# Kernel optimization log

Hardware: AMD Instinct MI355X
Metric: run time of the kernel (lower is better)

## Reference

```python
import jax, jax.numpy as jnp
import numpy as np

BITWIDTH = 4  # sqllm 4-bit packing: 8 codes per int32


def sqllm_dequant4(qweight, lut):
    # qweight: [num_int32s, N] int32 (stored packed); lut: [N, 16]
    qw = qweight.T  # [N, num_int32s]
    shifts = jnp.arange(8, dtype=jnp.int32) * 4  # [8]
    # extract 8 nibbles per int32 -> indices in [0, 16)
    idx = (qw[:, :, None] >> shifts[None, None, :]) & 15  # [N, num_int32s, 8]
    N = qw.shape[0]
    idx = idx.reshape(N, -1)  # [N, K] with K = num_int32s * 8
    return jnp.take_along_axis(lut, idx, axis=1)  # [N, K]


def setup_inputs() -> dict:
    key = jax.random.key(0)
    k1, k2, k3 = jax.random.split(key, 3)
    B, S, K, N = 4, 2048, 4096, 4096
    inp = {
        "input": jax.random.normal(k1, (B, S, K), dtype=jnp.float32),
        "qweight": jax.random.randint(k2, (K // 8, N), 0, 2147483647, dtype=jnp.int32),
        "lut": jax.random.normal(k3, (N, 16), dtype=jnp.float32),
    }
    return inp


def reference(input, qweight, lut):
    # sqllm_gemm: dequantize packed 4-bit weights via LUT gather, then input @ W.T
    weights = sqllm_dequant4(qweight, lut)  # [N, K]
    return jnp.einsum("bsk,nk->bsn", input, weights)  # [B, S, N]
```

## Files before the change

### kernel.cpp

```cpp
#include <hip/hip_runtime.h>
#include <hip/hip_bf16.h>


typedef __attribute__((ext_vector_type(4))) float  f32x4;
typedef __attribute__((ext_vector_type(4))) int    i32x4;
typedef __attribute__((ext_vector_type(8))) short  bf16x8;

__device__ __forceinline__ unsigned short f2bf(float f) {
    __hip_bfloat16 h = __float2bfloat16(f);
    return __builtin_bit_cast(unsigned short, h);
}

__device__ __forceinline__ void gload16(const unsigned short* g, unsigned short* l) {
    __builtin_amdgcn_global_load_lds(
        (const __attribute__((address_space(1))) unsigned int*)g,
        (__attribute__((address_space(3))) unsigned int*)l, 16, 0, 0);
}


__global__ void convA_kernel(const float* __restrict__ in, unsigned short* __restrict__ o, long n8) {
    long i = (long)blockIdx.x * blockDim.x + threadIdx.x;
    long stride = (long)gridDim.x * blockDim.x;
    const f32x4* in4 = reinterpret_cast<const f32x4*>(in);
    bf16x8* o8 = reinterpret_cast<bf16x8*>(o);
    for (; i < n8; i += stride) {
        f32x4 a = in4[2 * i];
        f32x4 b = in4[2 * i + 1];
        bf16x8 e;
#pragma unroll
        for (int x = 0; x < 4; ++x) {
            e[x]     = (short)f2bf(a[x]);
            e[4 + x] = (short)f2bf(b[x]);
        }
        o8[i] = e;
    }
}

__global__ void dequantW_kernel(const int* __restrict__ Q, const float* __restrict__ lut,
                                unsigned short* __restrict__ Wb, int N, long total) {
    long i = (long)blockIdx.x * blockDim.x + threadIdx.x;
    if (i >= total) return;
    unsigned int v = (unsigned int)Q[i];
    int n = (int)(i % N);
    const float* lp = lut + (long)n * 16;
    bf16x8 w;
#pragma unroll
    for (int p = 0; p < 8; ++p)
        w[p] = (short)f2bf(lp[(v >> (4 * p)) & 15]);
    reinterpret_cast<bf16x8*>(Wb)[i] = w;
}


#define MFMA4(MF, AF) \
    acc[MF][0] = __builtin_amdgcn_mfma_f32_16x16x32_bf16(AF, bv0, acc[MF][0], 0, 0, 0); \
    acc[MF][1] = __builtin_amdgcn_mfma_f32_16x16x32_bf16(AF, bv1, acc[MF][1], 0, 0, 0); \
    acc[MF][2] = __builtin_amdgcn_mfma_f32_16x16x32_bf16(AF, bv2, acc[MF][2], 0, 0, 0); \
    acc[MF][3] = __builtin_amdgcn_mfma_f32_16x16x32_bf16(AF, bv3, acc[MF][3], 0, 0, 0);

__global__ __launch_bounds__(512, 2)
void gemm8p(const unsigned short* __restrict__ Abf, const unsigned short* __restrict__ Wb,
            float* __restrict__ out, int M, int N, int K) {
    __shared__ __align__(16) unsigned short sA[4 * 8192];
    __shared__ __align__(16) unsigned short sB[4 * 8192];

    const int tid  = threadIdx.x;
    const int lane = tid & 63;
    const int wid  = tid >> 6;
    const int wr   = wid >> 2;
    const int wc   = wid & 3;
    const int r15  = lane & 15;
    const int hi   = lane >> 4;

    int nwg = gridDim.x, orig = blockIdx.x;
    int wg = ((nwg & 7) == 0) ? (orig & 7) * (nwg >> 3) + (orig >> 3) : orig;
    const int NBN = N / 256;
    const int m0 = (wg / NBN) * 256, n0 = (wg % NBN) * 256;

    const int NH = K / 32;

    const int aoff = (wr * 128 + r15) * 32 + ((hi ^ ((r15 >> 1) & 3)) << 3);
    const int boff = hi * 2048 + (wc * 64 + r15) * 8;

    const int am  = tid >> 2, akc = tid & 3;
    const int akcs = (akc ^ ((am >> 1) & 3)) << 3;
    const unsigned short* baseA0 = Abf + (size_t)(m0 + am) * K + akcs;
    const unsigned short* baseA1 = Abf + (size_t)(m0 + am + 128) * K + akcs;
    const int bkc = tid >> 8, bn = tid & 255;
    const unsigned short* baseB0 = Wb + ((size_t)bkc * N + n0 + bn) * 8;
    const unsigned short* baseB1 = Wb + ((size_t)(bkc + 2) * N + n0 + bn) * 8;
    const size_t bstride = (size_t)32 * N;
    unsigned short* const dA = sA + wid * 512;
    unsigned short* const dB = sB + wid * 512;

    auto stage = [&](int S, int slot) {
        gload16(baseA0 + S * 32, dA + slot * 8192);
        gload16(baseB0 + S * bstride, dB + slot * 8192);
        gload16(baseA1 + S * 32, dA + slot * 8192 + 4096);
        gload16(baseB1 + S * bstride, dB + slot * 8192 + 4096);
    };

    f32x4 acc[8][4] = {};

    stage(0, 0);
    stage(1, 1);
    stage(2, 2);
    asm volatile("s_waitcnt vmcnt(8)" ::: "memory");
    __builtin_amdgcn_s_barrier();

#define PHASE(U) do {                                                             \
    const unsigned short* SA = sA + (U) * 8192;                                   \
    const unsigned short* SB = sB + (U) * 8192;                                   \
    int S = H + (U) + 3; if (S >= NH) S -= NH;                                    \
    stage(S, ((U) + 3) & 3);                                                      \
    bf16x8 bv0 = *(const bf16x8*)(SB + boff + 0 * 128);                           \
    bf16x8 bv1 = *(const bf16x8*)(SB + boff + 1 * 128);                           \
    bf16x8 bv2 = *(const bf16x8*)(SB + boff + 2 * 128);                           \
    bf16x8 bv3 = *(const bf16x8*)(SB + boff + 3 * 128);                           \
    bf16x8 a0 = *(const bf16x8*)(SA + aoff + 0 * 512);                            \
    bf16x8 a1 = *(const bf16x8*)(SA + aoff + 1 * 512);                            \
    __builtin_amdgcn_s_setprio(1);                                                \
    bf16x8 a2 = *(const bf16x8*)(SA + aoff + 2 * 512);                            \
    bf16x8 a3 = *(const bf16x8*)(SA + aoff + 3 * 512);                            \
    MFMA4(0, a0)                                                                  \
    MFMA4(1, a1)                                                                  \
    bf16x8 a4 = *(const bf16x8*)(SA + aoff + 4 * 512);                            \
    bf16x8 a5 = *(const bf16x8*)(SA + aoff + 5 * 512);                            \
    MFMA4(2, a2)                                                                  \
    MFMA4(3, a3)                                                                  \
    bf16x8 a6 = *(const bf16x8*)(SA + aoff + 6 * 512);                            \
    bf16x8 a7 = *(const bf16x8*)(SA + aoff + 7 * 512);                            \
    MFMA4(4, a4)                                                                  \
    MFMA4(5, a5)                                                                  \
    MFMA4(6, a6)                                                                  \
    MFMA4(7, a7)                                                                  \
    __builtin_amdgcn_s_setprio(0);                                                \
    asm volatile("s_waitcnt vmcnt(8)" ::: "memory");                              \
    __builtin_amdgcn_s_barrier();                                                 \
} while (0)

    for (int H = 0; H < NH; H += 4) {
        PHASE(0);
        PHASE(1);
        PHASE(2);
        PHASE(3);
    }
#undef PHASE

    asm volatile("s_waitcnt vmcnt(0)" ::: "memory");

#pragma unroll
    for (int mf = 0; mf < 8; ++mf) {
        const int mrow = m0 + wr * 128 + mf * 16 + hi * 4;
#pragma unroll
        for (int nf = 0; nf < 4; ++nf) {
            const int ncol = n0 + wc * 64 + nf * 16 + r15;
            float* po = out + (size_t)mrow * N + ncol;
#pragma unroll
            for (int r = 0; r < 4; ++r) po[(size_t)r * N] = acc[mf][nf][r];
        }
    }
}


#define FBM 128
#define FBN 128
#define FBK 64

__device__ __forceinline__ int fswz(int row, int kb) {
    return row * (FBK * 2) + (kb ^ ((row & 7) << 4));
}

__global__ __launch_bounds__(256, 2)
void sqllm_gemm_fused(const float* __restrict__ A, const int* __restrict__ Q,
                      const float* __restrict__ lut, float* __restrict__ out,
                      int M, int N, int K) {
    __shared__ __align__(16) char sA[FBM * FBK * 2];
    __shared__ __align__(16) char sB[FBN * FBK * 2];
    __shared__ float sLut[FBN * 17];

    const int tid  = threadIdx.x;
    const int lane = tid & 63;
    const int wid  = tid >> 6;
    const int wr   = wid >> 1;
    const int wc   = wid & 1;
    const int n0 = blockIdx.x * FBN;
    const int m0 = blockIdx.y * FBM;

    for (int i = tid; i < FBN * 16; i += 256) {
        int n = i >> 4, c = i & 15;
        sLut[n * 17 + c] = lut[(long)(n0 + n) * 16 + c];
    }
    __syncthreads();

    f32x4 acc[4][4] = {};
    const int nK = K / FBK;
    for (int kk = 0; kk < nK; ++kk) {
        {
            const int r = tid >> 1, h = tid & 1;
            const float* ap = A + (long)(m0 + r) * K + kk * FBK + h * 32;
            f32x4 v[8];
#pragma unroll
            for (int j = 0; j < 8; ++j) v[j] = reinterpret_cast<const f32x4*>(ap)[j];
            const int kr = tid >> 5, nq = (tid & 31) << 2;
            const int* qp = Q + (long)(kk * (FBK / 8) + kr) * N + n0 + nq;
            i32x4 q = *reinterpret_cast<const i32x4*>(qp);
#pragma unroll
            for (int j = 0; j < 4; ++j) {
                bf16x8 e;
#pragma unroll
                for (int x = 0; x < 4; ++x) {
                    e[x]     = (short)f2bf(v[2 * j][x]);
                    e[4 + x] = (short)f2bf(v[2 * j + 1][x]);
                }
                *reinterpret_cast<bf16x8*>(sA + fswz(r, h * 64 + j * 16)) = e;
            }
#pragma unroll
            for (int c = 0; c < 4; ++c) {
                const int n = nq + c;
                const float* lp = sLut + n * 17;
                unsigned int qq = (unsigned int)q[c];
                bf16x8 w;
#pragma unroll
                for (int p = 0; p < 8; ++p)
                    w[p] = (short)f2bf(lp[(qq >> (4 * p)) & 15]);
                *reinterpret_cast<bf16x8*>(sB + fswz(n, kr * 16)) = w;
            }
        }
        __syncthreads();
#pragma unroll
        for (int kh = 0; kh < 2; ++kh) {
            const int kb = kh * 64 + (lane >> 4) * 16;
            bf16x8 af[4], bfv[4];
#pragma unroll
            for (int i = 0; i < 4; ++i) {
                af[i]  = *reinterpret_cast<const bf16x8*>(sA + fswz(wr * 64 + i * 16 + (lane & 15), kb));
                bfv[i] = *reinterpret_cast<const bf16x8*>(sB + fswz(wc * 64 + i * 16 + (lane & 15), kb));
            }
#pragma unroll
            for (int i = 0; i < 4; ++i)
#pragma unroll
                for (int j = 0; j < 4; ++j)
                    acc[i][j] = __builtin_amdgcn_mfma_f32_16x16x32_bf16(af[i], bfv[j], acc[i][j], 0, 0, 0);
        }
        __syncthreads();
    }
    const int col = lane & 15;
    const int r4  = (lane >> 4) * 4;
#pragma unroll
    for (int i = 0; i < 4; ++i) {
        const int mrow = m0 + wr * 64 + i * 16 + r4;
#pragma unroll
        for (int j = 0; j < 4; ++j) {
            const int ncol = n0 + wc * 64 + j * 16 + col;
#pragma unroll
            for (int r = 0; r < 4; ++r)
                out[(long)(mrow + r) * N + ncol] = acc[i][j][r];
        }
    }
}

extern "C" void kernel_launch(void* const* d_in, const int* in_sizes, int n_in,
                              void* d_out, int out_size, void* d_ws, size_t ws_size,
                              hipStream_t stream) {
    const float* A   = (const float*)d_in[0];
    const int*   Q   = (const int*)d_in[1];
    const float* lut = (const float*)d_in[2];
    float* out = (float*)d_out;

    const long szA = in_sizes[0], szQ = in_sizes[1], szL = in_sizes[2];
    const int N = (int)(szL / 16);
    const int K = (int)(szQ * 8 / N);
    const int M = (int)(szA / K);

    const size_t needA = (size_t)M * K * 2;
    const size_t needW = (size_t)K * N * 2;

    const bool shape_ok = (M % 256 == 0) && (N % 256 == 0) && (K % 128 == 0);

    if (shape_ok && ws_size >= needA + needW) {
        unsigned short* Abf = (unsigned short*)d_ws;
        unsigned short* Wb  = (unsigned short*)((char*)d_ws + needA);
        const long n8 = (long)M * K / 8;
        convA_kernel<<<2048, 256, 0, stream>>>(A, Abf, n8);
        const long tq = (long)(K / 8) * N;
        dequantW_kernel<<<(int)((tq + 255) / 256), 256, 0, stream>>>(Q, lut, Wb, N, tq);
        dim3 grid((M / 256) * (N / 256));
        gemm8p<<<grid, 512, 0, stream>>>(Abf, Wb, out, M, N, K);
    } else {
        dim3 grid(N / FBN, M / FBM);
        sqllm_gemm_fused<<<grid, 256, 0, stream>>>(A, Q, lut, out, M, N, K);
    }
}
```

Measured before the change: 295.7 us.

## Double-buffer LDS fragments in registers to overlap with MFMA

Restructures the GEMM main loop so each phase loads the next slot's A/B fragments from LDS into a second register set while MFMAs run on the current set. It aims to hide LDS read latency behind matrix math. The global-load wait is tightened so the next slot is ready one phase earlier, which reduces effective prefetch depth. It roughly doubles fragment register usage, risking spills or lower occupancy.

```diff
diff --git a/kernel.cpp b/kernel.cpp
--- a/kernel.cpp
+++ b/kernel.cpp
@@ -51,11 +51,31 @@
 }
 
 
-#define MFMA4(MF, AF) \
-    acc[MF][0] = __builtin_amdgcn_mfma_f32_16x16x32_bf16(AF, bv0, acc[MF][0], 0, 0, 0); \
-    acc[MF][1] = __builtin_amdgcn_mfma_f32_16x16x32_bf16(AF, bv1, acc[MF][1], 0, 0, 0); \
-    acc[MF][2] = __builtin_amdgcn_mfma_f32_16x16x32_bf16(AF, bv2, acc[MF][2], 0, 0, 0); \
-    acc[MF][3] = __builtin_amdgcn_mfma_f32_16x16x32_bf16(AF, bv3, acc[MF][3], 0, 0, 0);
+#define LOADFRAGS(NA, NB, SLOT) do {                                              \
+    const unsigned short* SA_ = sA + (SLOT) * 8192;                               \
+    const unsigned short* SB_ = sB + (SLOT) * 8192;                               \
+    _Pragma("unroll") for (int nf = 0; nf < 4; ++nf)                              \
+        NB[nf] = *(const bf16x8*)(SB_ + boff + nf * 128);                         \
+    _Pragma("unroll") for (int mf = 0; mf < 8; ++mf)                              \
+        NA[mf] = *(const bf16x8*)(SA_ + aoff + mf * 512);                         \
+} while (0)
+
+#define MFMABLOCK(CA, CB)                                                         \
+    _Pragma("unroll") for (int mf = 0; mf < 8; ++mf)                              \
+        _Pragma("unroll") for (int nf = 0; nf < 4; ++nf)                          \
+            acc[mf][nf] = __builtin_amdgcn_mfma_f32_16x16x32_bf16(                \
+                CA[mf], CB[nf], acc[mf][nf], 0, 0, 0);
+
+#define PHASE(U, CA, CB, NA, NB) do {                                             \
+    int S = H + (U) + 3; if (S >= NH) S -= NH;                                    \
+    stage(S, ((U) + 3) & 3);                                                      \
+    LOADFRAGS(NA, NB, ((U) + 1) & 3);                                             \
+    __builtin_amdgcn_s_setprio(1);                                                \
+    MFMABLOCK(CA, CB)                                                             \
+    __builtin_amdgcn_s_setprio(0);                                                \
+    asm volatile("s_waitcnt vmcnt(4)" ::: "memory");                              \
+    __builtin_amdgcn_s_barrier();                                                 \
+} while (0)
 
 __global__ __launch_bounds__(512, 2)
 void gemm8p(const unsigned short* __restrict__ Abf, const unsigned short* __restrict__ Wb,
@@ -100,51 +120,21 @@
     };
 
     f32x4 acc[8][4] = {};
+    bf16x8 avA[8], bvA[4], avB[8], bvB[4];
 
     stage(0, 0);
     stage(1, 1);
     stage(2, 2);
-    asm volatile("s_waitcnt vmcnt(8)" ::: "memory");
+    asm volatile("s_waitcnt vmcnt(4)" ::: "memory");
     __builtin_amdgcn_s_barrier();
-
-#define PHASE(U) do {                                                             \
-    const unsigned short* SA = sA + (U) * 8192;                                   \
-    const unsigned short* SB = sB + (U) * 8192;                                   \
-    int S = H + (U) + 3; if (S >= NH) S -= NH;                                    \
-    stage(S, ((U) + 3) & 3);                                                      \
-    bf16x8 bv0 = *(const bf16x8*)(SB + boff + 0 * 128);                           \
-    bf16x8 bv1 = *(const bf16x8*)(SB + boff + 1 * 128);                           \
-    bf16x8 bv2 = *(const bf16x8*)(SB + boff + 2 * 128);                           \
-    bf16x8 bv3 = *(const bf16x8*)(SB + boff + 3 * 128);                           \
-    bf16x8 a0 = *(const bf16x8*)(SA + aoff + 0 * 512);                            \
-    bf16x8 a1 = *(const bf16x8*)(SA + aoff + 1 * 512);                            \
-    __builtin_amdgcn_s_setprio(1);                                                \
-    bf16x8 a2 = *(const bf16x8*)(SA + aoff + 2 * 512);                            \
-    bf16x8 a3 = *(const bf16x8*)(SA + aoff + 3 * 512);                            \
-    MFMA4(0, a0)                                                                  \
-    MFMA4(1, a1)                                                                  \
-    bf16x8 a4 = *(const bf16x8*)(SA + aoff + 4 * 512);                            \
-    bf16x8 a5 = *(const bf16x8*)(SA + aoff + 5 * 512);                            \
-    MFMA4(2, a2)                                                                  \
-    MFMA4(3, a3)                                                                  \
-    bf16x8 a6 = *(const bf16x8*)(SA + aoff + 6 * 512);                            \
-    bf16x8 a7 = *(const bf16x8*)(SA + aoff + 7 * 512);                            \
-    MFMA4(4, a4)                                                                  \
-    MFMA4(5, a5)                                                                  \
-    MFMA4(6, a6)                                                                  \
-    MFMA4(7, a7)                                                                  \
-    __builtin_amdgcn_s_setprio(0);                                                \
-    asm volatile("s_waitcnt vmcnt(8)" ::: "memory");                              \
-    __builtin_amdgcn_s_barrier();                                                 \
-} while (0)
+    LOADFRAGS(avA, bvA, 0);
 
     for (int H = 0; H < NH; H += 4) {
-        PHASE(0);
-        PHASE(1);
-        PHASE(2);
-        PHASE(3);
-    }
-#undef PHASE
+        PHASE(0, avA, bvA, avB, bvB);
+        PHASE(1, avB, bvB, avA, bvA);
+        PHASE(2, avA, bvA, avB, bvB);
+        PHASE(3, avB, bvB, avA, bvA);
+    }
 
     asm volatile("s_waitcnt vmcnt(0)" ::: "memory");
 
@@ -160,6 +150,10 @@
         }
     }
 }
+
+#undef PHASE
+#undef MFMABLOCK
+#undef LOADFRAGS
 
 
 #define FBM 128
```

Result: no change. 294.0 us (-0.6%).
